# Kernel optimization log

Measured on AMD Instinct MI355X. Metric: run time of the kernel, lower is better.

## Reference

```python
import jax, jax.numpy as jnp
import numpy as np

HIDDEN = 1024
ARC = 500
BATCH = 16
SEQ = 512


def setup_inputs() -> dict:
    key = jax.random.key(0)
    ks = jax.random.split(key, 12)
    s_h = 1.0 / np.sqrt(HIDDEN)
    s_a = 1.0 / np.sqrt(ARC)
    return {
        "hidden_states": jax.random.normal(ks[0], (BATCH, SEQ, HIDDEN), dtype=jnp.float32),
        # head MLP: Linear(hidden->arc), ReLU, (Dropout eval=identity), Linear(arc->arc)
        "w1h": jax.random.uniform(ks[1], (ARC, HIDDEN), jnp.float32, -s_h, s_h),
        "b1h": jax.random.uniform(ks[2], (ARC,), jnp.float32, -s_h, s_h),
        "w2h": jax.random.uniform(ks[3], (ARC, ARC), jnp.float32, -s_a, s_a),
        "b2h": jax.random.uniform(ks[4], (ARC,), jnp.float32, -s_a, s_a),
        # dep MLP
        "w1d": jax.random.uniform(ks[5], (ARC, HIDDEN), jnp.float32, -s_h, s_h),
        "b1d": jax.random.uniform(ks[6], (ARC,), jnp.float32, -s_h, s_h),
        "w2d": jax.random.uniform(ks[7], (ARC, ARC), jnp.float32, -s_a, s_a),
        "b2d": jax.random.uniform(ks[8], (ARC,), jnp.float32, -s_a, s_a),
        # nn.Bilinear(arc, arc, 1, bias=True): weight [1, arc, arc], bias [1]
        "Wb": jax.random.uniform(ks[9], (ARC, ARC), jnp.float32, -s_a, s_a),
        "bb": jax.random.uniform(ks[10], (1,), jnp.float32, -s_a, s_a),
    }


def reference(hidden_states, w1h, b1h, w2h, b2h, w1d, b1d, w2d, b2d, Wb, bb):
    # MLPs (dropout is identity at inference)
    head = jnp.maximum(hidden_states @ w1h.T + b1h, 0.0) @ w2h.T + b2h  # [B,S,A]
    dep = jnp.maximum(hidden_states @ w1d.T + b1d, 0.0) @ w2d.T + b2d  # [B,S,A]
    # seq_len <= 512 already; chunked bilinear == two GEMMs:
    # scores[b,i,j] = head[b,i] @ Wb @ dep[b,j] + bb
    headW = head @ Wb  # [B,S,A]
    arc_scores = jnp.einsum("bia,bja->bij", headW, dep) + bb[0]  # [B,S,S]
    return arc_scores
```

## Files before the change

kernel.cpp:

```cpp
#include <hip/hip_runtime.h>
#include <hip/hip_bf16.h>


#define HIDDEN 1024
#define ARC 500
#define AP 512
#define ROWS 8192

typedef __attribute__((ext_vector_type(4))) float f32x4;
typedef __attribute__((ext_vector_type(8))) short short8;

static __device__ __forceinline__ ushort f2bf(float f) {
  union { float f; unsigned u; } v; v.f = f;
  unsigned r = v.u + 0x7fffu + ((v.u >> 16) & 1u);
  return (ushort)(r >> 16);
}

__global__ void k_prep_all(const float* __restrict__ w1h, const float* __restrict__ b1h,
                           const float* __restrict__ w1d, const float* __restrict__ b1d,
                           const float* __restrict__ w2h, const float* __restrict__ b2h,
                           const float* __restrict__ w2d, const float* __restrict__ b2d,
                           const float* __restrict__ Wb, const float4* __restrict__ hs,
                           ushort* __restrict__ W1, ushort* __restrict__ WbT,
                           ushort* __restrict__ w2hT, ushort* __restrict__ W2,
                           float* __restrict__ b1c, ushort* __restrict__ hs_bf) {
  __shared__ float tlds[64 * 65];
  const int bid = blockIdx.x;
  const int tid = threadIdx.x;
  if (bid < 4096) {
    int idx = bid * 256 + tid;
    int n = idx >> 10, k = idx & 1023;
    float v = 0.f;
    if (n < ARC) v = w1h[(size_t)n * HIDDEN + k];
    else if (n >= AP && n < AP + ARC) v = w1d[(size_t)(n - AP) * HIDDEN + k];
    W1[idx] = f2bf(v);
  } else if (bid < 5120) {
    int idx = (bid - 4096) * 256 + tid;
    int n = idx >> 9, k = idx & 511;
    float v = 0.f;
    if (n < ARC) {
      if (k < ARC) v = w2d[(size_t)n * ARC + k];
      else if (k == 511) v = b2d[n];
    }
    W2[idx] = f2bf(v);
  } else if (bid < 5184) {
    const int tile = bid - 5120;
    const int ta = tile >> 3, tj = tile & 7;
#pragma unroll
    for (int i = 0; i < 16; ++i) {
      int e = i * 256 + tid;
      int jl = e >> 6, al = e & 63;
      int j = tj * 64 + jl, a = ta * 64 + al;
      tlds[jl * 65 + al] = (j < ARC && a < ARC) ? Wb[(size_t)j * ARC + a] : 0.f;
    }
    __syncthreads();
#pragma unroll
    for (int i = 0; i < 16; ++i) {
      int e = i * 256 + tid;
      int al = e >> 6, jl = e & 63;
      WbT[(size_t)(ta * 64 + al) * AP + tj * 64 + jl] = f2bf(tlds[jl * 65 + al]);
    }
  } else if (bid < 5248) {
    const int tile = bid - 5184;
    const int tk = tile >> 3, tj = tile & 7;
#pragma unroll
    for (int i = 0; i < 16; ++i) {
      int e = i * 256 + tid;
      int jl = e >> 6, kl = e & 63;
      int j = tj * 64 + jl, k = tk * 64 + kl;
      tlds[jl * 65 + kl] = (j < ARC && k < ARC) ? w2h[(size_t)j * ARC + k] : 0.f;
    }
    __syncthreads();
#pragma unroll
    for (int i = 0; i < 16; ++i) {
      int e = i * 256 + tid;
      int kl = e >> 6, jl = e & 63;
      int k = tk * 64 + kl, j = tj * 64 + jl;
      float v = tlds[jl * 65 + kl];
      if (k == 511) v = (j < ARC) ? b2h[j] : 0.f;
      w2hT[(size_t)k * AP + j] = f2bf(v);
    }
  } else if (bid < 5252) {
    int i = (bid - 5248) * 256 + tid;
    float v = 0.f;
    if (i < ARC) v = b1h[i];
    else if (i == 511 || i == 1023) v = 1.f;
    else if (i >= AP && i < AP + ARC) v = b1d[i - AP];
    b1c[i] = v;
  } else {
    const int n4 = ROWS * HIDDEN / 4;
    int i = (bid - 5252) * 256 + tid;
    for (; i < n4; i += 2048 * 256) {
      float4 v = hs[i];
      ushort4 o;
      o.x = f2bf(v.x); o.y = f2bf(v.y); o.z = f2bf(v.z); o.w = f2bf(v.w);
      *(ushort4*)(hs_bf + (size_t)i * 4) = o;
    }
  }
}

template <int BM, int BN>
__device__ __forceinline__ void gemm_body(
    const ushort* __restrict__ A, const ushort* __restrict__ B,
    const float* __restrict__ bias, int bias_mode,
    void* __restrict__ C, int out_bf16, int relu,
    int lda, int ldb, int ldc, int K, int tm, int tn, ushort* lds) {
  constexpr int WR = BM / 2, WCC = BN / 2;
  constexpr int MFR = WR / 16, NFR = WCC / 16;
  constexpr int CA = BM / 64, CB = BN / 64;
  constexpr int LPS = CA + CB;
  constexpr int BUFSZ = (BM + BN) * 32;

  const int t = threadIdx.x;
  const int w = t >> 6;
  const int l = t & 63;
  const int wr = w >> 1, wc = w & 1;

  f32x4 acc[MFR][NFR];
#pragma unroll
  for (int m = 0; m < MFR; ++m)
#pragma unroll
    for (int n = 0; n < NFR; ++n) acc[m][n] = f32x4{0.f, 0.f, 0.f, 0.f};

  const int srow = w * 16 + (l >> 2);
  const int scol = (((l & 3) ^ ((l >> 3) & 3))) * 8;
  const ushort* ag = A + (size_t)(tm + srow) * lda + scol;
  const ushort* bg = B + (size_t)(tn + srow) * ldb + scol;
  const int lofs = w * 512;

  const int fr = l & 15, fh = l >> 4;
  const int swz = (fr >> 1) & 3;
  const int fAo = (wr * WR + fr) * 32 + (fh ^ swz) * 8;
  const int fBo = (wc * WCC + fr) * 32 + (fh ^ swz) * 8;

  auto stage = [&](int kt, ushort* buf) {
#pragma unroll
    for (int c = 0; c < CA; ++c)
      __builtin_amdgcn_global_load_lds(
          (const __attribute__((address_space(1))) void*)(ag + (size_t)c * 64 * lda + kt),
          (__attribute__((address_space(3))) void*)(buf + lofs + c * 2048), 16, 0, 0);
#pragma unroll
    for (int c = 0; c < CB; ++c)
      __builtin_amdgcn_global_load_lds(
          (const __attribute__((address_space(1))) void*)(bg + (size_t)c * 64 * ldb + kt),
          (__attribute__((address_space(3))) void*)(buf + BM * 32 + lofs + c * 2048), 16, 0, 0);
  };
  auto compute = [&](const ushort* buf) {
    short8 af[MFR], bf[NFR];
#pragma unroll
    for (int m = 0; m < MFR; ++m) af[m] = *(const short8*)(buf + fAo + m * 16 * 32);
#pragma unroll
    for (int n = 0; n < NFR; ++n) bf[n] = *(const short8*)(buf + BM * 32 + fBo + n * 16 * 32);
#pragma unroll
    for (int m = 0; m < MFR; ++m)
#pragma unroll
      for (int n = 0; n < NFR; ++n)
        acc[m][n] = __builtin_amdgcn_mfma_f32_16x16x32_bf16(af[m], bf[n], acc[m][n], 0, 0, 0);
  };

  const int nt = K >> 5;
  stage(0, lds);
  stage(32, lds + BUFSZ);
  int cs = 0, ps = 2;
  for (int ti = 0; ti < nt; ++ti) {
    if (ti + 1 < nt) {
      if constexpr (LPS == 2)      asm volatile("s_waitcnt vmcnt(2)" ::: "memory");
      else if constexpr (LPS == 3) asm volatile("s_waitcnt vmcnt(3)" ::: "memory");
      else                         asm volatile("s_waitcnt vmcnt(4)" ::: "memory");
    } else {
      asm volatile("s_waitcnt vmcnt(0)" ::: "memory");
    }
    __builtin_amdgcn_s_barrier();
    __builtin_amdgcn_sched_barrier(0);
    if (ti + 2 < nt) stage((ti + 2) << 5, lds + ps * BUFSZ);
    __builtin_amdgcn_s_setprio(1);
    compute(lds + cs * BUFSZ);
    __builtin_amdgcn_s_setprio(0);
    cs = (cs == 2) ? 0 : cs + 1;
    ps = (ps == 2) ? 0 : ps + 1;
  }

  const int cr = fh * 4;
  const float bscal = (bias_mode == 2) ? bias[0] : 0.f;
#pragma unroll
  for (int m = 0; m < MFR; ++m) {
#pragma unroll
    for (int n = 0; n < NFR; ++n) {
      const int col = tn + wc * WCC + n * 16 + fr;
      const float bv = (bias_mode == 1) ? bias[col] : bscal;
#pragma unroll
      for (int j = 0; j < 4; ++j) {
        const int row = tm + wr * WR + m * 16 + cr + j;
        float v = acc[m][n][j] + bv;
        if (relu) v = fmaxf(v, 0.f);
        if (out_bf16)
          ((ushort*)C)[(size_t)row * ldc + col] = f2bf(v);
        else
          ((float*)C)[(size_t)row * ldc + col] = v;
      }
    }
  }
}

__global__ __launch_bounds__(256)
void k_g1mt(const ushort* __restrict__ hs_bf, const ushort* __restrict__ W1,
            const float* __restrict__ b1c, ushort* __restrict__ t1,
            const ushort* __restrict__ WbT, const ushort* __restrict__ w2hT,
            ushort* __restrict__ MTb) {
  __shared__ ushort lds[3 * (128 + 128) * 32];
  const int flat = blockIdx.y * 8 + blockIdx.x;
  const int f2 = (flat & 7) * 66 + (flat >> 3);
  const int by = f2 >> 3, bx = f2 & 7;
  if (by < 64) {
    gemm_body<128, 128>(hs_bf, W1, b1c, 1, t1, 1, 1,
                        HIDDEN, HIDDEN, 1024, HIDDEN, by * 128, bx * 128, lds);
  } else {
    const int idx = (by - 64) * 8 + bx;
    gemm_body<128, 128>(WbT, w2hT, nullptr, 0, MTb, 1, 0,
                        AP, AP, AP, AP, (idx >> 2) * 128, (idx & 3) * 128, lds);
  }
}

template <int BM, int BN>
__global__ __launch_bounds__(256)
void k_gemm_rt(const ushort* __restrict__ A, const ushort* __restrict__ B,
               const float* __restrict__ bias, int bias_mode,
               void* __restrict__ C, int out_bf16, int relu,
               int lda, int ldb, int ldc, int K,
               long aBS, long bBS, long cBS) {
  __shared__ ushort lds[3 * (BM + BN) * 32];
  const int gx = gridDim.x, gy = gridDim.y;
  const int gxy = gx * gy;
  const int nwg = gxy * gridDim.z;
  const int flat = (blockIdx.z * gy + blockIdx.y) * gx + blockIdx.x;
  const int q = nwg >> 3;
  const int f2 = (flat & 7) * q + (flat >> 3);
  const int bz = f2 / gxy;
  const int rm = f2 - bz * gxy;
  const int by = rm / gx;
  const int bx = rm - by * gx;

  const ushort* Az = A + (size_t)aBS * bz;
  const ushort* Bz = B + (size_t)bBS * bz;
  void* Cz = out_bf16 ? (void*)((ushort*)C + (size_t)cBS * bz)
                      : (void*)((float*)C + (size_t)cBS * bz);
  gemm_body<BM, BN>(Az, Bz, bias, bias_mode, Cz, out_bf16, relu,
                    lda, ldb, ldc, K, by * BM, bx * BN, lds);
}

extern "C" void kernel_launch(void* const* d_in, const int* in_sizes, int n_in,
                              void* d_out, int out_size, void* d_ws, size_t ws_size,
                              hipStream_t stream) {
  const float* hs  = (const float*)d_in[0];
  const float* w1h = (const float*)d_in[1];
  const float* b1h = (const float*)d_in[2];
  const float* w2h = (const float*)d_in[3];
  const float* b2h = (const float*)d_in[4];
  const float* w1d = (const float*)d_in[5];
  const float* b1d = (const float*)d_in[6];
  const float* w2d = (const float*)d_in[7];
  const float* b2d = (const float*)d_in[8];
  const float* Wb  = (const float*)d_in[9];
  const float* bb  = (const float*)d_in[10];

  char* ws = (char*)d_ws;
  ushort* hs_bf = (ushort*)(ws + 0);
  ushort* W1    = (ushort*)(ws + 16777216);
  ushort* WbT   = (ushort*)(ws + 18874368);
  ushort* w2hT  = (ushort*)(ws + 19398656);
  ushort* MT    = (ushort*)(ws + 19922944);
  ushort* W2    = (ushort*)(ws + 20447232);
  ushort* t1    = (ushort*)(ws + 20971520);
  ushort* hw    = (ushort*)(ws + 37748736);
  float*  b1c   = (float*)(ws + 54525952);
  float*  out   = (float*)d_out;

  k_prep_all<<<7300, 256, 0, stream>>>(w1h, b1h, w1d, b1d, w2h, b2h, w2d, b2d,
                                       Wb, (const float4*)hs,
                                       W1, WbT, w2hT, W2, b1c, hs_bf);

  k_g1mt<<<dim3(8, 66), 256, 0, stream>>>(hs_bf, W1, b1c, t1, WbT, w2hT, MT);

  k_gemm_rt<128, 128><<<dim3(4, 64, 2), 256, 0, stream>>>(
      t1, MT, nullptr, 0, hw, 1, 0, 1024, AP, AP, AP,
      AP, (long)AP * AP, (long)ROWS * AP);

  k_gemm_rt<128, 64><<<dim3(8, 4, 16), 256, 0, stream>>>(
      hw, hw + (size_t)ROWS * AP, bb, 2, out, 0, 0, AP, AP, 512, AP,
      (long)512 * AP, (long)512 * AP, (long)512 * 512);
}
```

Baseline: 163.8 us.

## Fuse all stages into one persistent kernel with grid-wide atomic barriers

Replaces four separate launches (prep, first GEMM plus MT, second GEMM, final batched GEMM) with a single persistent kernel of 512 blocks that loops over the prep work and separates the stages with a software grid barrier built on an atomic counter. The MT product switches to 64x64 tiles run by the first 64 blocks alongside the main GEMM tiles. The aim is to remove kernel launch gaps and tail effects between stages. The risks are spin-wait overhead, imbalance because the MT blocks do extra work, reliance on all 512 blocks being co-resident to avoid deadlock, and an extra memset launch to reset the counter.

```diff
diff --git a/kernel.cpp b/kernel.cpp
--- a/kernel.cpp
+++ b/kernel.cpp
@@ -6,6 +6,7 @@
 #define ARC 500
 #define AP 512
 #define ROWS 8192
+#define NB 512
 
 typedef __attribute__((ext_vector_type(4))) float f32x4;
 typedef __attribute__((ext_vector_type(8))) short short8;
@@ -16,87 +17,15 @@
   return (ushort)(r >> 16);
 }
 
-__global__ void k_prep_all(const float* __restrict__ w1h, const float* __restrict__ b1h,
-                           const float* __restrict__ w1d, const float* __restrict__ b1d,
-                           const float* __restrict__ w2h, const float* __restrict__ b2h,
-                           const float* __restrict__ w2d, const float* __restrict__ b2d,
-                           const float* __restrict__ Wb, const float4* __restrict__ hs,
-                           ushort* __restrict__ W1, ushort* __restrict__ WbT,
-                           ushort* __restrict__ w2hT, ushort* __restrict__ W2,
-                           float* __restrict__ b1c, ushort* __restrict__ hs_bf) {
-  __shared__ float tlds[64 * 65];
-  const int bid = blockIdx.x;
-  const int tid = threadIdx.x;
-  if (bid < 4096) {
-    int idx = bid * 256 + tid;
-    int n = idx >> 10, k = idx & 1023;
-    float v = 0.f;
-    if (n < ARC) v = w1h[(size_t)n * HIDDEN + k];
-    else if (n >= AP && n < AP + ARC) v = w1d[(size_t)(n - AP) * HIDDEN + k];
-    W1[idx] = f2bf(v);
-  } else if (bid < 5120) {
-    int idx = (bid - 4096) * 256 + tid;
-    int n = idx >> 9, k = idx & 511;
-    float v = 0.f;
-    if (n < ARC) {
-      if (k < ARC) v = w2d[(size_t)n * ARC + k];
-      else if (k == 511) v = b2d[n];
-    }
-    W2[idx] = f2bf(v);
-  } else if (bid < 5184) {
-    const int tile = bid - 5120;
-    const int ta = tile >> 3, tj = tile & 7;
-#pragma unroll
-    for (int i = 0; i < 16; ++i) {
-      int e = i * 256 + tid;
-      int jl = e >> 6, al = e & 63;
-      int j = tj * 64 + jl, a = ta * 64 + al;
-      tlds[jl * 65 + al] = (j < ARC && a < ARC) ? Wb[(size_t)j * ARC + a] : 0.f;
-    }
-    __syncthreads();
-#pragma unroll
-    for (int i = 0; i < 16; ++i) {
-      int e = i * 256 + tid;
-      int al = e >> 6, jl = e & 63;
-      WbT[(size_t)(ta * 64 + al) * AP + tj * 64 + jl] = f2bf(tlds[jl * 65 + al]);
-    }
-  } else if (bid < 5248) {
-    const int tile = bid - 5184;
-    const int tk = tile >> 3, tj = tile & 7;
-#pragma unroll
-    for (int i = 0; i < 16; ++i) {
-      int e = i * 256 + tid;
-      int jl = e >> 6, kl = e & 63;
-      int j = tj * 64 + jl, k = tk * 64 + kl;
-      tlds[jl * 65 + kl] = (j < ARC && k < ARC) ? w2h[(size_t)j * ARC + k] : 0.f;
-    }
-    __syncthreads();
-#pragma unroll
-    for (int i = 0; i < 16; ++i) {
-      int e = i * 256 + tid;
-      int kl = e >> 6, jl = e & 63;
-      int k = tk * 64 + kl, j = tj * 64 + jl;
-      float v = tlds[jl * 65 + kl];
-      if (k == 511) v = (j < ARC) ? b2h[j] : 0.f;
-      w2hT[(size_t)k * AP + j] = f2bf(v);
-    }
-  } else if (bid < 5252) {
-    int i = (bid - 5248) * 256 + tid;
-    float v = 0.f;
-    if (i < ARC) v = b1h[i];
-    else if (i == 511 || i == 1023) v = 1.f;
-    else if (i >= AP && i < AP + ARC) v = b1d[i - AP];
-    b1c[i] = v;
-  } else {
-    const int n4 = ROWS * HIDDEN / 4;
-    int i = (bid - 5252) * 256 + tid;
-    for (; i < n4; i += 2048 * 256) {
-      float4 v = hs[i];
-      ushort4 o;
-      o.x = f2bf(v.x); o.y = f2bf(v.y); o.z = f2bf(v.z); o.w = f2bf(v.w);
-      *(ushort4*)(hs_bf + (size_t)i * 4) = o;
-    }
-  }
+static __device__ __forceinline__ void gsync(unsigned* cnt, unsigned target) {
+  __syncthreads();
+  __threadfence();
+  if (threadIdx.x == 0) {
+    atomicAdd(cnt, 1u);
+    while (atomicAdd(cnt, 0u) < target) __builtin_amdgcn_s_sleep(2);
+  }
+  __syncthreads();
+  __threadfence();
 }
 
 template <int BM, int BN>
@@ -202,50 +131,147 @@
   }
 }
 
+static __device__ void prep_unit(
+    int u, int tid, float* tlds,
+    const float* __restrict__ w1h, const float* __restrict__ b1h,
+    const float* __restrict__ w1d, const float* __restrict__ b1d,
+    const float* __restrict__ w2h, const float* __restrict__ b2h,
+    const float* __restrict__ w2d, const float* __restrict__ b2d,
+    const float* __restrict__ Wb, const float4* __restrict__ hs,
+    ushort* __restrict__ W1, ushort* __restrict__ WbT,
+    ushort* __restrict__ w2hT, ushort* __restrict__ W2,
+    float* __restrict__ b1c, ushort* __restrict__ hs_bf) {
+  if (u < 4096) {
+    int idx = u * 256 + tid;
+    int n = idx >> 10, k = idx & 1023;
+    float v = 0.f;
+    if (n < ARC) v = w1h[(size_t)n * HIDDEN + k];
+    else if (n >= AP && n < AP + ARC) v = w1d[(size_t)(n - AP) * HIDDEN + k];
+    W1[idx] = f2bf(v);
+  } else if (u < 5120) {
+    int idx = (u - 4096) * 256 + tid;
+    int n = idx >> 9, k = idx & 511;
+    float v = 0.f;
+    if (n < ARC) {
+      if (k < ARC) v = w2d[(size_t)n * ARC + k];
+      else if (k == 511) v = b2d[n];
+    }
+    W2[idx] = f2bf(v);
+  } else if (u < 5184) {
+    const int tile = u - 5120;
+    const int ta = tile >> 3, tj = tile & 7;
+#pragma unroll
+    for (int i = 0; i < 16; ++i) {
+      int e = i * 256 + tid;
+      int jl = e >> 6, al = e & 63;
+      int j = tj * 64 + jl, a = ta * 64 + al;
+      tlds[jl * 65 + al] = (j < ARC && a < ARC) ? Wb[(size_t)j * ARC + a] : 0.f;
+    }
+    __syncthreads();
+#pragma unroll
+    for (int i = 0; i < 16; ++i) {
+      int e = i * 256 + tid;
+      int al = e >> 6, jl = e & 63;
+      WbT[(size_t)(ta * 64 + al) * AP + tj * 64 + jl] = f2bf(tlds[jl * 65 + al]);
+    }
+    __syncthreads();
+  } else if (u < 5248) {
+    const int tile = u - 5184;
+    const int tk = tile >> 3, tj = tile & 7;
+#pragma unroll
+    for (int i = 0; i < 16; ++i) {
+      int e = i * 256 + tid;
+      int jl = e >> 6, kl = e & 63;
+      int j = tj * 64 + jl, k = tk * 64 + kl;
+      tlds[jl * 65 + kl] = (j < ARC && k < ARC) ? w2h[(size_t)j * ARC + k] : 0.f;
+    }
+    __syncthreads();
+#pragma unroll
+    for (int i = 0; i < 16; ++i) {
+      int e = i * 256 + tid;
+      int kl = e >> 6, jl = e & 63;
+      int k = tk * 64 + kl, j = tj * 64 + jl;
+      float v = tlds[jl * 65 + kl];
+      if (k == 511) v = (j < ARC) ? b2h[j] : 0.f;
+      w2hT[(size_t)k * AP + j] = f2bf(v);
+    }
+    __syncthreads();
+  } else if (u < 5252) {
+    int i = (u - 5248) * 256 + tid;
+    float v = 0.f;
+    if (i < ARC) v = b1h[i];
+    else if (i == 511 || i == 1023) v = 1.f;
+    else if (i >= AP && i < AP + ARC) v = b1d[i - AP];
+    b1c[i] = v;
+  } else {
+    const int n4 = ROWS * HIDDEN / 4;
+    for (int i = (u - 5252) * 256 + tid; i < n4; i += 2048 * 256) {
+      float4 v = hs[i];
+      ushort4 o;
+      o.x = f2bf(v.x); o.y = f2bf(v.y); o.z = f2bf(v.z); o.w = f2bf(v.w);
+      *(ushort4*)(hs_bf + (size_t)i * 4) = o;
+    }
+  }
+}
+
 __global__ __launch_bounds__(256)
-void k_g1mt(const ushort* __restrict__ hs_bf, const ushort* __restrict__ W1,
-            const float* __restrict__ b1c, ushort* __restrict__ t1,
-            const ushort* __restrict__ WbT, const ushort* __restrict__ w2hT,
-            ushort* __restrict__ MTb) {
+void k_fused(const float* __restrict__ w1h, const float* __restrict__ b1h,
+             const float* __restrict__ w2h, const float* __restrict__ b2h,
+             const float* __restrict__ w1d, const float* __restrict__ b1d,
+             const float* __restrict__ w2d, const float* __restrict__ b2d,
+             const float* __restrict__ Wb, const float* __restrict__ bb,
+             const float4* __restrict__ hs,
+             ushort* __restrict__ hs_bf, ushort* __restrict__ W1,
+             ushort* __restrict__ WbT, ushort* __restrict__ w2hT,
+             ushort* __restrict__ MT, ushort* __restrict__ W2,
+             ushort* __restrict__ t1, ushort* __restrict__ hw,
+             float* __restrict__ b1c, float* __restrict__ out,
+             unsigned* __restrict__ barcnt) {
   __shared__ ushort lds[3 * (128 + 128) * 32];
-  const int flat = blockIdx.y * 8 + blockIdx.x;
-  const int f2 = (flat & 7) * 66 + (flat >> 3);
-  const int by = f2 >> 3, bx = f2 & 7;
-  if (by < 64) {
+  const int b = blockIdx.x;
+  const int tid = threadIdx.x;
+
+  for (int u = b; u < 7300; u += NB)
+    prep_unit(u, tid, (float*)lds, w1h, b1h, w1d, b1d, w2h, b2h, w2d, b2d,
+              Wb, hs, W1, WbT, w2hT, W2, b1c, hs_bf);
+  gsync(barcnt, NB);
+
+  {
+    const int f2 = (b & 7) * 64 + (b >> 3);
+    const int by = f2 >> 3, bx = f2 & 7;
     gemm_body<128, 128>(hs_bf, W1, b1c, 1, t1, 1, 1,
                         HIDDEN, HIDDEN, 1024, HIDDEN, by * 128, bx * 128, lds);
-  } else {
-    const int idx = (by - 64) * 8 + bx;
-    gemm_body<128, 128>(WbT, w2hT, nullptr, 0, MTb, 1, 0,
-                        AP, AP, AP, AP, (idx >> 2) * 128, (idx & 3) * 128, lds);
-  }
-}
-
-template <int BM, int BN>
-__global__ __launch_bounds__(256)
-void k_gemm_rt(const ushort* __restrict__ A, const ushort* __restrict__ B,
-               const float* __restrict__ bias, int bias_mode,
-               void* __restrict__ C, int out_bf16, int relu,
-               int lda, int ldb, int ldc, int K,
-               long aBS, long bBS, long cBS) {
-  __shared__ ushort lds[3 * (BM + BN) * 32];
-  const int gx = gridDim.x, gy = gridDim.y;
-  const int gxy = gx * gy;
-  const int nwg = gxy * gridDim.z;
-  const int flat = (blockIdx.z * gy + blockIdx.y) * gx + blockIdx.x;
-  const int q = nwg >> 3;
-  const int f2 = (flat & 7) * q + (flat >> 3);
-  const int bz = f2 / gxy;
-  const int rm = f2 - bz * gxy;
-  const int by = rm / gx;
-  const int bx = rm - by * gx;
-
-  const ushort* Az = A + (size_t)aBS * bz;
-  const ushort* Bz = B + (size_t)bBS * bz;
-  void* Cz = out_bf16 ? (void*)((ushort*)C + (size_t)cBS * bz)
-                      : (void*)((float*)C + (size_t)cBS * bz);
-  gemm_body<BM, BN>(Az, Bz, bias, bias_mode, Cz, out_bf16, relu,
-                    lda, ldb, ldc, K, by * BM, bx * BN, lds);
+    if (b < 64) {
+      gemm_body<64, 64>(WbT, w2hT, nullptr, 0, MT, 1, 0,
+                        AP, AP, AP, AP, (b >> 3) * 64, (b & 7) * 64, lds);
+    }
+  }
+  gsync(barcnt, 2 * NB);
+
+  {
+    const int f2 = (b & 7) * 64 + (b >> 3);
+    const int z = f2 >> 8;
+    const int rm = f2 & 255;
+    const int by = rm >> 2, bx = rm & 3;
+    const ushort* Az = t1 + (size_t)z * AP;
+    const ushort* Bz = z ? W2 : MT;
+    ushort* Cz = hw + (size_t)z * ROWS * AP;
+    gemm_body<128, 128>(Az, Bz, nullptr, 0, Cz, 1, 0,
+                        1024, AP, AP, AP, by * 128, bx * 128, lds);
+  }
+  gsync(barcnt, 3 * NB);
+
+  {
+    const int f2 = (b & 7) * 64 + (b >> 3);
+    const int z = f2 >> 5;
+    const int tt = f2 & 31;
+    const int by = tt >> 3, bx = tt & 7;
+    const ushort* Az = hw + (size_t)z * 512 * AP;
+    const ushort* Bz = hw + (size_t)ROWS * AP + (size_t)z * 512 * AP;
+    float* Cz = out + (size_t)z * 512 * 512;
+    gemm_body<128, 64>(Az, Bz, bb, 2, Cz, 0, 0,
+                       AP, AP, 512, AP, by * 128, bx * 64, lds);
+  }
 }
 
 extern "C" void kernel_launch(void* const* d_in, const int* in_sizes, int n_in,
@@ -264,28 +290,21 @@
   const float* bb  = (const float*)d_in[10];
 
   char* ws = (char*)d_ws;
-  ushort* hs_bf = (ushort*)(ws + 0);
-  ushort* W1    = (ushort*)(ws + 16777216);
-  ushort* WbT   = (ushort*)(ws + 18874368);
-  ushort* w2hT  = (ushort*)(ws + 19398656);
-  ushort* MT    = (ushort*)(ws + 19922944);
-  ushort* W2    = (ushort*)(ws + 20447232);
-  ushort* t1    = (ushort*)(ws + 20971520);
-  ushort* hw    = (ushort*)(ws + 37748736);
-  float*  b1c   = (float*)(ws + 54525952);
-  float*  out   = (float*)d_out;
-
-  k_prep_all<<<7300, 256, 0, stream>>>(w1h, b1h, w1d, b1d, w2h, b2h, w2d, b2d,
-                                       Wb, (const float4*)hs,
-                                       W1, WbT, w2hT, W2, b1c, hs_bf);
-
-  k_g1mt<<<dim3(8, 66), 256, 0, stream>>>(hs_bf, W1, b1c, t1, WbT, w2hT, MT);
-
-  k_gemm_rt<128, 128><<<dim3(4, 64, 2), 256, 0, stream>>>(
-      t1, MT, nullptr, 0, hw, 1, 0, 1024, AP, AP, AP,
-      AP, (long)AP * AP, (long)ROWS * AP);
-
-  k_gemm_rt<128, 64><<<dim3(8, 4, 16), 256, 0, stream>>>(
-      hw, hw + (size_t)ROWS * AP, bb, 2, out, 0, 0, AP, AP, 512, AP,
-      (long)512 * AP, (long)512 * AP, (long)512 * 512);
-}
+  ushort*   hs_bf = (ushort*)(ws + 0);
+  ushort*   W1    = (ushort*)(ws + 16777216);
+  ushort*   WbT   = (ushort*)(ws + 18874368);
+  ushort*   w2hT  = (ushort*)(ws + 19398656);
+  ushort*   MT    = (ushort*)(ws + 19922944);
+  ushort*   W2    = (ushort*)(ws + 20447232);
+  ushort*   t1    = (ushort*)(ws + 20971520);
+  ushort*   hw    = (ushort*)(ws + 37748736);
+  float*    b1c   = (float*)(ws + 54525952);
+  unsigned* bar   = (unsigned*)(ws + 54530048);
+  float*    out   = (float*)d_out;
+
+  hipMemsetAsync(bar, 0, 4, stream);
+  k_fused<<<NB, 256, 0, stream>>>(w1h, b1h, w2h, b2h, w1d, b1d, w2d, b2d,
+                                  Wb, bb, (const float4*)hs,
+                                  hs_bf, W1, WbT, w2hT, MT, W2, t1, hw,
+                                  b1c, out, bar);
+}
```

After: 540.0 us. 3.3x slower.
